# Kernel optimization log

Hardware: AMD Instinct MI355X
Metric: run time of the kernel (lower is better)

Reference implementation:

```python
import jax, jax.numpy as jnp
import numpy as np

N_NODES = 50000
N_EDGES = 600000
D_FEAT = 128
HIDDEN = 128
OUT = 64


def sage_conv(x, src, dst, Wl, bl, Wr, n_nodes):
    # message = x[src] gathered per edge; mean-aggregated at dst
    msg = x[src]                                            # [E, d]
    agg = jax.ops.segment_sum(msg, dst, num_segments=n_nodes)   # [N, d]
    cnt = jax.ops.segment_sum(jnp.ones((src.shape[0],), x.dtype), dst,
                              num_segments=n_nodes)             # [N]
    mean = agg / jnp.maximum(cnt, 1.0)[:, None]
    # PyG SAGEConv: lin_l(mean_neighbors) + lin_r(x_root); only lin_l has bias
    return mean @ Wl + bl + x @ Wr


def setup_inputs() -> dict:
    key = jax.random.key(0)
    ks = jax.random.split(key, 7)
    x = jax.random.normal(ks[0], (N_NODES, D_FEAT), dtype=jnp.float32)
    edge_index = jax.random.randint(ks[1], (2, N_EDGES), 0, N_NODES, dtype=jnp.int64)
    s1 = 1.0 / np.sqrt(D_FEAT)
    s2 = 1.0 / np.sqrt(HIDDEN)
    W1l = jax.random.normal(ks[2], (D_FEAT, HIDDEN), dtype=jnp.float32) * s1
    b1l = jnp.zeros((HIDDEN,), dtype=jnp.float32)
    W1r = jax.random.normal(ks[3], (D_FEAT, HIDDEN), dtype=jnp.float32) * s1
    W2l = jax.random.normal(ks[4], (HIDDEN, OUT), dtype=jnp.float32) * s2
    b2l = jnp.zeros((OUT,), dtype=jnp.float32)
    W2r = jax.random.normal(ks[5], (HIDDEN, OUT), dtype=jnp.float32) * s2
    return {"x": x, "edge_index": edge_index, "W1l": W1l, "b1l": b1l,
            "W1r": W1r, "W2l": W2l, "b2l": b2l, "W2r": W2r}


def reference(x, edge_index, W1l, b1l, W1r, W2l, b2l, W2r):
    n = x.shape[0]
    src, dst = edge_index[0], edge_index[1]
    h = sage_conv(x, src, dst, W1l, b1l, W1r, n)
    h = jax.nn.relu(h)
    out = sage_conv(h, src, dst, W2l, b2l, W2r, n)
    return out
```

## Files before the change

### kernel.cpp

```cpp
#include <hip/hip_runtime.h>
#include <cstdint>
#include <cstddef>

#define D 128
#define O2 64
#define PAD 136
#define CAP 64

typedef __attribute__((ext_vector_type(8))) short bf16x8;
typedef __attribute__((ext_vector_type(4))) float f32x4;

__device__ inline unsigned short f2bf(float f) {
  union { float f; uint32_t u; } v; v.f = f;
  uint32_t r = v.u + 0x7FFF + ((v.u >> 16) & 1);
  return (unsigned short)(r >> 16);
}
__device__ inline float bf_lo(uint32_t w) {
  union { uint32_t u; float f; } v; v.u = w << 16; return v.f;
}
__device__ inline float bf_hi(uint32_t w) {
  union { uint32_t u; float f; } v; v.u = w & 0xFFFF0000u; return v.f;
}

__device__ __forceinline__ void gather16(
    const unsigned short* __restrict__ xb, const unsigned short* __restrict__ bucket,
    int cnt, int j, float a[16])
{
  int p = 0;
  for (; p + 8 <= cnt; p += 8) {
    uint4 bi = *(const uint4*)(bucket + p);
    int s[8];
    s[0] = bi.x & 0xFFFF; s[1] = bi.x >> 16;
    s[2] = bi.y & 0xFFFF; s[3] = bi.y >> 16;
    s[4] = bi.z & 0xFFFF; s[5] = bi.z >> 16;
    s[6] = bi.w & 0xFFFF; s[7] = bi.w >> 16;
    uint4 v0[8], v1[8];
    #pragma unroll
    for (int q = 0; q < 8; q++) {
      const unsigned short* r = xb + (size_t)s[q] * 128 + j * 16;
      v0[q] = *(const uint4*)r;
      v1[q] = *(const uint4*)(r + 8);
    }
    #pragma unroll
    for (int q = 0; q < 8; q++) {
      a[0]+=bf_lo(v0[q].x); a[1]+=bf_hi(v0[q].x);
      a[2]+=bf_lo(v0[q].y); a[3]+=bf_hi(v0[q].y);
      a[4]+=bf_lo(v0[q].z); a[5]+=bf_hi(v0[q].z);
      a[6]+=bf_lo(v0[q].w); a[7]+=bf_hi(v0[q].w);
      a[8]+=bf_lo(v1[q].x); a[9]+=bf_hi(v1[q].x);
      a[10]+=bf_lo(v1[q].y); a[11]+=bf_hi(v1[q].y);
      a[12]+=bf_lo(v1[q].z); a[13]+=bf_hi(v1[q].z);
      a[14]+=bf_lo(v1[q].w); a[15]+=bf_hi(v1[q].w);
    }
  }
  for (; p + 4 <= cnt; p += 4) {
    uint2 bi = *(const uint2*)(bucket + p);
    int s[4];
    s[0] = bi.x & 0xFFFF; s[1] = bi.x >> 16;
    s[2] = bi.y & 0xFFFF; s[3] = bi.y >> 16;
    uint4 v0[4], v1[4];
    #pragma unroll
    for (int q = 0; q < 4; q++) {
      const unsigned short* r = xb + (size_t)s[q] * 128 + j * 16;
      v0[q] = *(const uint4*)r;
      v1[q] = *(const uint4*)(r + 8);
    }
    #pragma unroll
    for (int q = 0; q < 4; q++) {
      a[0]+=bf_lo(v0[q].x); a[1]+=bf_hi(v0[q].x);
      a[2]+=bf_lo(v0[q].y); a[3]+=bf_hi(v0[q].y);
      a[4]+=bf_lo(v0[q].z); a[5]+=bf_hi(v0[q].z);
      a[6]+=bf_lo(v0[q].w); a[7]+=bf_hi(v0[q].w);
      a[8]+=bf_lo(v1[q].x); a[9]+=bf_hi(v1[q].x);
      a[10]+=bf_lo(v1[q].y); a[11]+=bf_hi(v1[q].y);
      a[12]+=bf_lo(v1[q].z); a[13]+=bf_hi(v1[q].z);
      a[14]+=bf_lo(v1[q].w); a[15]+=bf_hi(v1[q].w);
    }
  }
  for (; p < cnt; p++) {
    const unsigned short* rA = xb + (size_t)bucket[p] * 128 + j * 16;
    uint4 vA0 = *(const uint4*)rA, vA1 = *(const uint4*)(rA + 8);
    a[0]+=bf_lo(vA0.x); a[1]+=bf_hi(vA0.x); a[2]+=bf_lo(vA0.y); a[3]+=bf_hi(vA0.y);
    a[4]+=bf_lo(vA0.z); a[5]+=bf_hi(vA0.z); a[6]+=bf_lo(vA0.w); a[7]+=bf_hi(vA0.w);
    a[8]+=bf_lo(vA1.x); a[9]+=bf_hi(vA1.x); a[10]+=bf_lo(vA1.y); a[11]+=bf_hi(vA1.y);
    a[12]+=bf_lo(vA1.z); a[13]+=bf_hi(vA1.z); a[14]+=bf_lo(vA1.w); a[15]+=bf_hi(vA1.w);
  }
}

__global__ __launch_bounds__(256) void prep_all(
    const int* __restrict__ src, const int* __restrict__ dst,
    int* __restrict__ deg, unsigned short* __restrict__ eidx, int n_edges,
    const float* __restrict__ x, const float* __restrict__ W1l,
    const float* __restrict__ W1r, const float* __restrict__ W2l,
    const float* __restrict__ W2r, unsigned short* __restrict__ xb,
    unsigned short* __restrict__ WT1, unsigned short* __restrict__ WT2,
    int n_nodes, int edge_blocks, int xb_blocks)
{
  int b = blockIdx.x;
  if (b < edge_blocks) {
    const int half = n_edges >> 1;
    int e = b * 256 + threadIdx.x;
    if (e < half) {
      int d0 = dst[e],        d1 = dst[e + half];
      int s0 = src[e],        s1 = src[e + half];
      int p0 = atomicAdd(&deg[d0], 1);
      int p1 = atomicAdd(&deg[d1], 1);
      if (p0 < CAP)
        __builtin_nontemporal_store((unsigned short)s0, eidx + (size_t)d0 * CAP + p0);
      if (p1 < CAP)
        __builtin_nontemporal_store((unsigned short)s1, eidx + (size_t)d1 * CAP + p1);
    }
  } else if (b < edge_blocks + xb_blocks) {
    int i = (b - edge_blocks) * 256 + threadIdx.x;
    if (i < n_nodes * 32) {
      int n = i >> 5, q = i & 31;
      float4 v = ((const float4*)x)[(size_t)n * 32 + q];
      unsigned long long o =
          (unsigned long long)f2bf(v.x)
        | ((unsigned long long)f2bf(v.y) << 16)
        | ((unsigned long long)f2bf(v.z) << 32)
        | ((unsigned long long)f2bf(v.w) << 48);
      __builtin_nontemporal_store(o, (unsigned long long*)(xb + (size_t)n * 128 + q * 4));
    }
  } else {
    int t = (b - edge_blocks - xb_blocks) * 256 + threadIdx.x;
    if (t < 128 * 256) {
      int n = t >> 8, k = t & 255;
      float w = (k < 128) ? W1l[(size_t)k * 128 + n] : W1r[(size_t)(k - 128) * 128 + n];
      WT1[t] = f2bf(w);
    } else {
      int u = t - 128 * 256;
      if (u < 128 * 128) {
        int n = u >> 7, k = u & 127;
        float w = (n < 64) ? W2l[(size_t)k * 64 + n] : W2r[(size_t)k * 64 + (n - 64)];
        WT2[u] = f2bf(w);
      }
    }
  }
}

__global__ __launch_bounds__(256, 2) void fused_l12(
    const unsigned short* __restrict__ xb, const unsigned short* __restrict__ eidx,
    const int* __restrict__ deg, const unsigned short* __restrict__ WT1,
    const unsigned short* __restrict__ WT2, const float* __restrict__ b1l,
    unsigned short* __restrict__ hl, float* __restrict__ outp, int n_nodes)
{
  __shared__ unsigned short s_m[128 * PAD];
  const int NB0 = blockIdx.x * 128;

  {
    const int j = threadIdx.x & 7;
    const int g = threadIdx.x >> 3;
    #pragma unroll 1
    for (int pass = 0; pass < 4; pass++) {
      const int nl = pass * 32 + g;
      const int n = NB0 + nl;
      float a[16];
      #pragma unroll
      for (int i = 0; i < 16; i++) a[i] = 0.f;
      float ic = 0.f;
      if (n < n_nodes) {
        const int dg = deg[n];
        const int cnt = min(dg, CAP);
        gather16(xb, eidx + (size_t)n * CAP, cnt, j, a);
        ic = 1.0f / fmaxf((float)dg, 1.0f);
      }
      uint4 o0, o1;
      o0.x = ((uint32_t)f2bf(a[1]*ic) << 16) | f2bf(a[0]*ic);
      o0.y = ((uint32_t)f2bf(a[3]*ic) << 16) | f2bf(a[2]*ic);
      o0.z = ((uint32_t)f2bf(a[5]*ic) << 16) | f2bf(a[4]*ic);
      o0.w = ((uint32_t)f2bf(a[7]*ic) << 16) | f2bf(a[6]*ic);
      o1.x = ((uint32_t)f2bf(a[9]*ic) << 16) | f2bf(a[8]*ic);
      o1.y = ((uint32_t)f2bf(a[11]*ic) << 16) | f2bf(a[10]*ic);
      o1.z = ((uint32_t)f2bf(a[13]*ic) << 16) | f2bf(a[12]*ic);
      o1.w = ((uint32_t)f2bf(a[15]*ic) << 16) | f2bf(a[14]*ic);
      unsigned short* mr = s_m + nl * PAD + j * 16;
      *(uint4*)mr = o0;
      *(uint4*)(mr + 8) = o1;
    }
  }
  __syncthreads();

  const int lane = threadIdx.x & 63;
  const int w    = threadIdx.x >> 6;
  const int quad = lane >> 4, l15 = lane & 15;
  const int N0 = NB0 + w * 32;
  const int ra0 = min(N0 + l15, n_nodes - 1);
  const int ra1 = min(N0 + 16 + l15, n_nodes - 1);

  const unsigned short* sm0 = s_m + (w * 32 + l15) * PAD + quad * 8;
  const unsigned short* sm1 = sm0 + 16 * PAD;

  bf16x8 af[2][8];
  #pragma unroll
  for (int s = 0; s < 4; s++) {
    af[0][s]     = *(const bf16x8*)(sm0 + s * 32);
    af[1][s]     = *(const bf16x8*)(sm1 + s * 32);
    af[0][s + 4] = *(const bf16x8*)(xb + (size_t)ra0 * 128 + quad * 8 + s * 32);
    af[1][s + 4] = *(const bf16x8*)(xb + (size_t)ra1 * 128 + quad * 8 + s * 32);
  }

  f32x4 acc[2][8];
  #pragma unroll
  for (int rt = 0; rt < 2; rt++)
    #pragma unroll
    for (int tt = 0; tt < 8; tt++) acc[rt][tt] = (f32x4){0.f, 0.f, 0.f, 0.f};

  const unsigned short* b1 = WT1 + (size_t)l15 * 256 + quad * 8;
  bf16x8 cur[8], nxt[8];
  #pragma unroll
  for (int s = 0; s < 8; s++) cur[s] = *(const bf16x8*)(b1 + s * 32);
  #pragma unroll
  for (int tt = 0; tt < 8; tt++) {
    if (tt < 7) {
      #pragma unroll
      for (int s = 0; s < 8; s++)
        nxt[s] = *(const bf16x8*)(b1 + (size_t)(tt + 1) * 16 * 256 + s * 32);
    }
    #pragma unroll
    for (int s = 0; s < 8; s++) {
      acc[0][tt] = __builtin_amdgcn_mfma_f32_16x16x32_bf16(af[0][s], cur[s], acc[0][tt], 0, 0, 0);
      acc[1][tt] = __builtin_amdgcn_mfma_f32_16x16x32_bf16(af[1][s], cur[s], acc[1][tt], 0, 0, 0);
    }
    #pragma unroll
    for (int s = 0; s < 8; s++) cur[s] = nxt[s];
  }

  unsigned short* s_hw = s_m + (size_t)w * 32 * PAD;
  #pragma unroll
  for (int tt = 0; tt < 8; tt++) {
    int col = tt * 16 + l15;
    float bias = b1l[col];
    #pragma unroll
    for (int rt = 0; rt < 2; rt++) {
      int rb = rt * 16 + quad * 4;
      #pragma unroll
      for (int r = 0; r < 4; r++)
        s_hw[(rb + r) * PAD + col] = f2bf(fmaxf(acc[rt][tt][r] + bias, 0.f));
    }
  }

  bf16x8 af2[2][4];
  #pragma unroll
  for (int s = 0; s < 4; s++) {
    af2[0][s] = *(const bf16x8*)(s_hw + (l15)      * PAD + quad * 8 + s * 32);
    af2[1][s] = *(const bf16x8*)(s_hw + (16 + l15) * PAD + quad * 8 + s * 32);
  }
  f32x4 acc2[2][8];
  #pragma unroll
  for (int rt = 0; rt < 2; rt++)
    #pragma unroll
    for (int tt = 0; tt < 8; tt++) acc2[rt][tt] = (f32x4){0.f, 0.f, 0.f, 0.f};

  const unsigned short* b2 = WT2 + (size_t)l15 * 128 + quad * 8;
  bf16x8 cur2[4], nxt2[4];
  #pragma unroll
  for (int s = 0; s < 4; s++) cur2[s] = *(const bf16x8*)(b2 + s * 32);
  #pragma unroll
  for (int tt = 0; tt < 8; tt++) {
    if (tt < 7) {
      #pragma unroll
      for (int s = 0; s < 4; s++)
        nxt2[s] = *(const bf16x8*)(b2 + (size_t)(tt + 1) * 16 * 128 + s * 32);
    }
    #pragma unroll
    for (int s = 0; s < 4; s++) {
      acc2[0][tt] = __builtin_amdgcn_mfma_f32_16x16x32_bf16(af2[0][s], cur2[s], acc2[0][tt], 0, 0, 0);
      acc2[1][tt] = __builtin_amdgcn_mfma_f32_16x16x32_bf16(af2[1][s], cur2[s], acc2[1][tt], 0, 0, 0);
    }
    #pragma unroll
    for (int s = 0; s < 4; s++) cur2[s] = nxt2[s];
  }

  #pragma unroll
  for (int tt = 0; tt < 8; tt++) {
    int col = tt * 16 + l15;
    #pragma unroll
    for (int rt = 0; rt < 2; rt++) {
      int rowb = N0 + rt * 16 + quad * 4;
      #pragma unroll
      for (int r = 0; r < 4; r++) {
        int row = rowb + r;
        if (row < n_nodes) {
          if (tt < 4) hl[(size_t)row * 64 + col] = f2bf(acc2[rt][tt][r]);
          else        outp[(size_t)row * 64 + (col - 64)] = acc2[rt][tt][r];
        }
      }
    }
  }
}

__global__ __launch_bounds__(256) void gather2_kernel(
    const unsigned short* __restrict__ hl, const unsigned short* __restrict__ eidx,
    const int* __restrict__ deg, const float* __restrict__ b2l,
    float* __restrict__ out, int n_nodes)
{
  const int j = threadIdx.x & 7;
  const int g = threadIdx.x >> 3;
  const int n = blockIdx.x * 32 + g;
  if (n >= n_nodes) return;
  const int dg = deg[n];
  const int cnt = min(dg, CAP);
  const unsigned short* bucket = eidx + (size_t)n * CAP;
  float a[8];
  #pragma unroll
  for (int i = 0; i < 8; i++) a[i] = 0.f;
  int p = 0;
  for (; p + 8 <= cnt; p += 8) {
    uint4 bi = *(const uint4*)(bucket + p);
    int s[8];
    s[0] = bi.x & 0xFFFF; s[1] = bi.x >> 16;
    s[2] = bi.y & 0xFFFF; s[3] = bi.y >> 16;
    s[4] = bi.z & 0xFFFF; s[5] = bi.z >> 16;
    s[6] = bi.w & 0xFFFF; s[7] = bi.w >> 16;
    uint4 v[8];
    #pragma unroll
    for (int q = 0; q < 8; q++)
      v[q] = *(const uint4*)(hl + (size_t)s[q] * 64 + j * 8);
    #pragma unroll
    for (int q = 0; q < 8; q++) {
      a[0]+=bf_lo(v[q].x); a[1]+=bf_hi(v[q].x);
      a[2]+=bf_lo(v[q].y); a[3]+=bf_hi(v[q].y);
      a[4]+=bf_lo(v[q].z); a[5]+=bf_hi(v[q].z);
      a[6]+=bf_lo(v[q].w); a[7]+=bf_hi(v[q].w);
    }
  }
  for (; p + 4 <= cnt; p += 4) {
    uint2 bi = *(const uint2*)(bucket + p);
    int s[4];
    s[0] = bi.x & 0xFFFF; s[1] = bi.x >> 16;
    s[2] = bi.y & 0xFFFF; s[3] = bi.y >> 16;
    uint4 v[4];
    #pragma unroll
    for (int q = 0; q < 4; q++)
      v[q] = *(const uint4*)(hl + (size_t)s[q] * 64 + j * 8);
    #pragma unroll
    for (int q = 0; q < 4; q++) {
      a[0]+=bf_lo(v[q].x); a[1]+=bf_hi(v[q].x);
      a[2]+=bf_lo(v[q].y); a[3]+=bf_hi(v[q].y);
      a[4]+=bf_lo(v[q].z); a[5]+=bf_hi(v[q].z);
      a[6]+=bf_lo(v[q].w); a[7]+=bf_hi(v[q].w);
    }
  }
  for (; p < cnt; p++) {
    uint4 vA = *(const uint4*)(hl + (size_t)bucket[p] * 64 + j * 8);
    a[0]+=bf_lo(vA.x); a[1]+=bf_hi(vA.x); a[2]+=bf_lo(vA.y); a[3]+=bf_hi(vA.y);
    a[4]+=bf_lo(vA.z); a[5]+=bf_hi(vA.z); a[6]+=bf_lo(vA.w); a[7]+=bf_hi(vA.w);
  }
  const float ic = 1.0f / fmaxf((float)dg, 1.0f);
  float* o = out + (size_t)n * 64 + j * 8;
  const float* bb = b2l + j * 8;
  float4 p0 = *(const float4*)(o);
  float4 p1 = *(const float4*)(o + 4);
  p0.x += bb[0] + a[0] * ic; p0.y += bb[1] + a[1] * ic;
  p0.z += bb[2] + a[2] * ic; p0.w += bb[3] + a[3] * ic;
  p1.x += bb[4] + a[4] * ic; p1.y += bb[5] + a[5] * ic;
  p1.z += bb[6] + a[6] * ic; p1.w += bb[7] + a[7] * ic;
  *(float4*)(o) = p0;
  *(float4*)(o + 4) = p1;
}

extern "C" void kernel_launch(void* const* d_in, const int* in_sizes, int n_in,
                              void* d_out, int out_size, void* d_ws, size_t ws_size,
                              hipStream_t stream)
{
  const float* x   = (const float*)d_in[0];
  const int*   ei  = (const int*)d_in[1];
  const float* W1l = (const float*)d_in[2];
  const float* b1l = (const float*)d_in[3];
  const float* W1r = (const float*)d_in[4];
  const float* W2l = (const float*)d_in[5];
  const float* b2l = (const float*)d_in[6];
  const float* W2r = (const float*)d_in[7];
  float* out = (float*)d_out;

  const int n_nodes = in_sizes[0] / D;
  const int n_edges = in_sizes[1] / 2;
  const int* src = ei;
  const int* dst = ei + n_edges;

  char* ws = (char*)d_ws;
  auto align256 = [](size_t v) { return (v + 255) & ~(size_t)255; };
  const size_t szN = align256((size_t)n_nodes * 4);

  size_t o = 0;
  int* deg = (int*)(ws + o);  o += szN;
  unsigned short* eidx = (unsigned short*)(ws + o); o += align256((size_t)n_nodes * CAP * 2);
  unsigned short* WT1  = (unsigned short*)(ws + o); o += align256(128 * 256 * 2);
  unsigned short* WT2  = (unsigned short*)(ws + o); o += align256(128 * 128 * 2);
  unsigned short* xb   = (unsigned short*)(ws + o); o += align256((size_t)n_nodes * 128 * 2);
  unsigned short* hl   = (unsigned short*)(ws + o); o += align256((size_t)n_nodes * 64 * 2);

  hipMemsetAsync(deg, 0, szN, stream);

  const int half = n_edges >> 1;
  const int edge_blocks = (half + 255) / 256;
  const int xb_blocks = (n_nodes * 32 + 255) / 256;
  const int w_blocks  = (128 * 256 + 128 * 128 + 255) / 256;

  prep_all<<<edge_blocks + xb_blocks + w_blocks, 256, 0, stream>>>(
      src, dst, deg, eidx, n_edges,
      x, W1l, W1r, W2l, W2r, xb, WT1, WT2, n_nodes, edge_blocks, xb_blocks);

  fused_l12<<<(n_nodes + 127) / 128, 256, 0, stream>>>(
      xb, eidx, deg, WT1, WT2, b1l, hl, out, n_nodes);

  gather2_kernel<<<(n_nodes + 31) / 32, 256, 0, stream>>>(
      hl, eidx, deg, b2l, out, n_nodes);
}
```

Measured before the change: 194.9 us.

## Shrink fused layer block to 32 nodes and split output columns across waves

The fused layer kernel now handles 32 nodes per block instead of 128, so the gather runs as a single pass and there are four times as many blocks. The four waves are arranged as two row groups times two column halves, which adds a block barrier between the two GEMMs because a row's hidden values now come from two waves. The weight double-buffering is removed and occupancy is raised to 5 blocks per CU through smaller shared memory and fewer registers. The goal is more latency hiding for the irregular gather, at the cost of loading weights more often per node and an extra sync.

```diff
diff --git a/kernel.cpp b/kernel.cpp
--- a/kernel.cpp
+++ b/kernel.cpp
@@ -139,152 +139,112 @@
   }
 }
 
-__global__ __launch_bounds__(256, 2) void fused_l12(
+__global__ __launch_bounds__(256, 5) void fused_l12(
     const unsigned short* __restrict__ xb, const unsigned short* __restrict__ eidx,
     const int* __restrict__ deg, const unsigned short* __restrict__ WT1,
     const unsigned short* __restrict__ WT2, const float* __restrict__ b1l,
     unsigned short* __restrict__ hl, float* __restrict__ outp, int n_nodes)
 {
-  __shared__ unsigned short s_m[128 * PAD];
-  const int NB0 = blockIdx.x * 128;
+  __shared__ unsigned short s_m[32 * PAD];
+  __shared__ unsigned short s_h[32 * PAD];
+  const int NB0 = blockIdx.x * 32;
 
   {
     const int j = threadIdx.x & 7;
     const int g = threadIdx.x >> 3;
-    #pragma unroll 1
-    for (int pass = 0; pass < 4; pass++) {
-      const int nl = pass * 32 + g;
-      const int n = NB0 + nl;
-      float a[16];
-      #pragma unroll
-      for (int i = 0; i < 16; i++) a[i] = 0.f;
-      float ic = 0.f;
-      if (n < n_nodes) {
-        const int dg = deg[n];
-        const int cnt = min(dg, CAP);
-        gather16(xb, eidx + (size_t)n * CAP, cnt, j, a);
-        ic = 1.0f / fmaxf((float)dg, 1.0f);
-      }
-      uint4 o0, o1;
-      o0.x = ((uint32_t)f2bf(a[1]*ic) << 16) | f2bf(a[0]*ic);
-      o0.y = ((uint32_t)f2bf(a[3]*ic) << 16) | f2bf(a[2]*ic);
-      o0.z = ((uint32_t)f2bf(a[5]*ic) << 16) | f2bf(a[4]*ic);
-      o0.w = ((uint32_t)f2bf(a[7]*ic) << 16) | f2bf(a[6]*ic);
-      o1.x = ((uint32_t)f2bf(a[9]*ic) << 16) | f2bf(a[8]*ic);
-      o1.y = ((uint32_t)f2bf(a[11]*ic) << 16) | f2bf(a[10]*ic);
-      o1.z = ((uint32_t)f2bf(a[13]*ic) << 16) | f2bf(a[12]*ic);
-      o1.w = ((uint32_t)f2bf(a[15]*ic) << 16) | f2bf(a[14]*ic);
-      unsigned short* mr = s_m + nl * PAD + j * 16;
-      *(uint4*)mr = o0;
-      *(uint4*)(mr + 8) = o1;
-    }
+    const int n = NB0 + g;
+    float a[16];
+    #pragma unroll
+    for (int i = 0; i < 16; i++) a[i] = 0.f;
+    float ic = 0.f;
+    if (n < n_nodes) {
+      const int dg = deg[n];
+      const int cnt = min(dg, CAP);
+      gather16(xb, eidx + (size_t)n * CAP, cnt, j, a);
+      ic = 1.0f / fmaxf((float)dg, 1.0f);
+    }
+    uint4 o0, o1;
+    o0.x = ((uint32_t)f2bf(a[1]*ic) << 16) | f2bf(a[0]*ic);
+    o0.y = ((uint32_t)f2bf(a[3]*ic) << 16) | f2bf(a[2]*ic);
+    o0.z = ((uint32_t)f2bf(a[5]*ic) << 16) | f2bf(a[4]*ic);
+    o0.w = ((uint32_t)f2bf(a[7]*ic) << 16) | f2bf(a[6]*ic);
+    o1.x = ((uint32_t)f2bf(a[9]*ic) << 16) | f2bf(a[8]*ic);
+    o1.y = ((uint32_t)f2bf(a[11]*ic) << 16) | f2bf(a[10]*ic);
+    o1.z = ((uint32_t)f2bf(a[13]*ic) << 16) | f2bf(a[12]*ic);
+    o1.w = ((uint32_t)f2bf(a[15]*ic) << 16) | f2bf(a[14]*ic);
+    unsigned short* mr = s_m + g * PAD + j * 16;
+    *(uint4*)mr = o0;
+    *(uint4*)(mr + 8) = o1;
   }
   __syncthreads();
 
   const int lane = threadIdx.x & 63;
   const int w    = threadIdx.x >> 6;
+  const int rg   = w >> 1;
+  const int ch   = w & 1;
   const int quad = lane >> 4, l15 = lane & 15;
-  const int N0 = NB0 + w * 32;
-  const int ra0 = min(N0 + l15, n_nodes - 1);
-  const int ra1 = min(N0 + 16 + l15, n_nodes - 1);
-
-  const unsigned short* sm0 = s_m + (w * 32 + l15) * PAD + quad * 8;
-  const unsigned short* sm1 = sm0 + 16 * PAD;
-
-  bf16x8 af[2][8];
+  const int N0 = NB0 + rg * 16;
+  const int ra = min(N0 + l15, n_nodes - 1);
+
+  bf16x8 af[8];
   #pragma unroll
   for (int s = 0; s < 4; s++) {
-    af[0][s]     = *(const bf16x8*)(sm0 + s * 32);
-    af[1][s]     = *(const bf16x8*)(sm1 + s * 32);
-    af[0][s + 4] = *(const bf16x8*)(xb + (size_t)ra0 * 128 + quad * 8 + s * 32);
-    af[1][s + 4] = *(const bf16x8*)(xb + (size_t)ra1 * 128 + quad * 8 + s * 32);
-  }
-
-  f32x4 acc[2][8];
-  #pragma unroll
-  for (int rt = 0; rt < 2; rt++)
-    #pragma unroll
-    for (int tt = 0; tt < 8; tt++) acc[rt][tt] = (f32x4){0.f, 0.f, 0.f, 0.f};
-
-  const unsigned short* b1 = WT1 + (size_t)l15 * 256 + quad * 8;
-  bf16x8 cur[8], nxt[8];
-  #pragma unroll
-  for (int s = 0; s < 8; s++) cur[s] = *(const bf16x8*)(b1 + s * 32);
-  #pragma unroll
-  for (int tt = 0; tt < 8; tt++) {
-    if (tt < 7) {
-      #pragma unroll
-      for (int s = 0; s < 8; s++)
-        nxt[s] = *(const bf16x8*)(b1 + (size_t)(tt + 1) * 16 * 256 + s * 32);
-    }
+    af[s]     = *(const bf16x8*)(s_m + (rg * 16 + l15) * PAD + quad * 8 + s * 32);
+    af[s + 4] = *(const bf16x8*)(xb + (size_t)ra * 128 + quad * 8 + s * 32);
+  }
+
+  f32x4 acc[4];
+  #pragma unroll
+  for (int tt = 0; tt < 4; tt++) acc[tt] = (f32x4){0.f, 0.f, 0.f, 0.f};
+
+  const unsigned short* b1 = WT1 + (size_t)(ch * 4) * 16 * 256 + (size_t)l15 * 256 + quad * 8;
+  #pragma unroll
+  for (int tt = 0; tt < 4; tt++) {
     #pragma unroll
     for (int s = 0; s < 8; s++) {
-      acc[0][tt] = __builtin_amdgcn_mfma_f32_16x16x32_bf16(af[0][s], cur[s], acc[0][tt], 0, 0, 0);
-      acc[1][tt] = __builtin_amdgcn_mfma_f32_16x16x32_bf16(af[1][s], cur[s], acc[1][tt], 0, 0, 0);
-    }
-    #pragma unroll
-    for (int s = 0; s < 8; s++) cur[s] = nxt[s];
-  }
-
-  unsigned short* s_hw = s_m + (size_t)w * 32 * PAD;
-  #pragma unroll
-  for (int tt = 0; tt < 8; tt++) {
-    int col = tt * 16 + l15;
+      bf16x8 bw = *(const bf16x8*)(b1 + (size_t)tt * 16 * 256 + s * 32);
+      acc[tt] = __builtin_amdgcn_mfma_f32_16x16x32_bf16(af[s], bw, acc[tt], 0, 0, 0);
+    }
+  }
+
+  #pragma unroll
+  for (int tt = 0; tt < 4; tt++) {
+    int col = (ch * 4 + tt) * 16 + l15;
     float bias = b1l[col];
     #pragma unroll
-    for (int rt = 0; rt < 2; rt++) {
-      int rb = rt * 16 + quad * 4;
-      #pragma unroll
-      for (int r = 0; r < 4; r++)
-        s_hw[(rb + r) * PAD + col] = f2bf(fmaxf(acc[rt][tt][r] + bias, 0.f));
-    }
-  }
-
-  bf16x8 af2[2][4];
-  #pragma unroll
-  for (int s = 0; s < 4; s++) {
-    af2[0][s] = *(const bf16x8*)(s_hw + (l15)      * PAD + quad * 8 + s * 32);
-    af2[1][s] = *(const bf16x8*)(s_hw + (16 + l15) * PAD + quad * 8 + s * 32);
-  }
-  f32x4 acc2[2][8];
-  #pragma unroll
-  for (int rt = 0; rt < 2; rt++)
-    #pragma unroll
-    for (int tt = 0; tt < 8; tt++) acc2[rt][tt] = (f32x4){0.f, 0.f, 0.f, 0.f};
-
-  const unsigned short* b2 = WT2 + (size_t)l15 * 128 + quad * 8;
-  bf16x8 cur2[4], nxt2[4];
-  #pragma unroll
-  for (int s = 0; s < 4; s++) cur2[s] = *(const bf16x8*)(b2 + s * 32);
-  #pragma unroll
-  for (int tt = 0; tt < 8; tt++) {
-    if (tt < 7) {
-      #pragma unroll
-      for (int s = 0; s < 4; s++)
-        nxt2[s] = *(const bf16x8*)(b2 + (size_t)(tt + 1) * 16 * 128 + s * 32);
-    }
+    for (int r = 0; r < 4; r++)
+      s_h[(rg * 16 + quad * 4 + r) * PAD + col] = f2bf(fmaxf(acc[tt][r] + bias, 0.f));
+  }
+  __syncthreads();
+
+  bf16x8 af2[4];
+  #pragma unroll
+  for (int s = 0; s < 4; s++)
+    af2[s] = *(const bf16x8*)(s_h + (rg * 16 + l15) * PAD + quad * 8 + s * 32);
+
+  f32x4 acc2[4];
+  #pragma unroll
+  for (int tt = 0; tt < 4; tt++) acc2[tt] = (f32x4){0.f, 0.f, 0.f, 0.f};
+
+  const unsigned short* b2 = WT2 + (size_t)(ch * 4) * 16 * 128 + (size_t)l15 * 128 + quad * 8;
+  #pragma unroll
+  for (int tt = 0; tt < 4; tt++) {
     #pragma unroll
     for (int s = 0; s < 4; s++) {
-      acc2[0][tt] = __builtin_amdgcn_mfma_f32_16x16x32_bf16(af2[0][s], cur2[s], acc2[0][tt], 0, 0, 0);
-      acc2[1][tt] = __builtin_amdgcn_mfma_f32_16x16x32_bf16(af2[1][s], cur2[s], acc2[1][tt], 0, 0, 0);
-    }
-    #pragma unroll
-    for (int s = 0; s < 4; s++) cur2[s] = nxt2[s];
-  }
-
-  #pragma unroll
-  for (int tt = 0; tt < 8; tt++) {
-    int col = tt * 16 + l15;
-    #pragma unroll
-    for (int rt = 0; rt < 2; rt++) {
-      int rowb = N0 + rt * 16 + quad * 4;
-      #pragma unroll
-      for (int r = 0; r < 4; r++) {
-        int row = rowb + r;
-        if (row < n_nodes) {
-          if (tt < 4) hl[(size_t)row * 64 + col] = f2bf(acc2[rt][tt][r]);
-          else        outp[(size_t)row * 64 + (col - 64)] = acc2[rt][tt][r];
-        }
+      bf16x8 bw = *(const bf16x8*)(b2 + (size_t)tt * 16 * 128 + s * 32);
+      acc2[tt] = __builtin_amdgcn_mfma_f32_16x16x32_bf16(af2[s], bw, acc2[tt], 0, 0, 0);
+    }
+  }
+
+  #pragma unroll
+  for (int tt = 0; tt < 4; tt++) {
+    int gcol = (ch * 4 + tt) * 16 + l15;
+    #pragma unroll
+    for (int r = 0; r < 4; r++) {
+      int row = N0 + quad * 4 + r;
+      if (row < n_nodes) {
+        if (ch == 0) hl[(size_t)row * 64 + gcol] = f2bf(acc2[tt][r]);
+        else         outp[(size_t)row * 64 + (gcol - 64)] = acc2[tt][r];
       }
     }
   }
@@ -402,7 +362,7 @@
       src, dst, deg, eidx, n_edges,
       x, W1l, W1r, W2l, W2r, xb, WT1, WT2, n_nodes, edge_blocks, xb_blocks);
 
-  fused_l12<<<(n_nodes + 127) / 128, 256, 0, stream>>>(
+  fused_l12<<<(n_nodes + 31) / 32, 256, 0, stream>>>(
       xb, eidx, deg, WT1, WT2, b1l, hl, out, n_nodes);
 
   gather2_kernel<<<(n_nodes + 31) / 32, 256, 0, stream>>>(
```

Measured after the change: 203.4 us. 1.04x slower.
